# Kernel tuning notes

Hardware: AMD Instinct MI355X
Metric: run time of the kernel (lower is better)

The kernel has to match this reference:

```python
import jax, jax.numpy as jnp
import numpy as np

N_NODES = 100000
N_EDGES = 600000
D_IN = 128
D_OUT = 128

def gcn_conv(x, src, dst, W, b, n):
    # PyG GCNConv: h = X W; out_i = sum_j norm_ij * h_j + b, with self-loops and
    # symmetric normalization norm_ij = deg_i^{-1/2} deg_j^{-1/2}.
    deg = jax.ops.segment_sum(jnp.ones_like(dst, dtype=x.dtype), dst, num_segments=n)
    dinv = jnp.where(deg > 0, jax.lax.rsqrt(deg), 0.0)
    norm = dinv[src] * dinv[dst]            # [E]
    h = x @ W                                # [N, D_out]
    msg = h[src] * norm[:, None]             # gather + scale, [E, D_out]
    out = jax.ops.segment_sum(msg, dst, num_segments=n)
    return out + b

def setup_inputs() -> dict:
    key = jax.random.key(0)
    ks = jax.random.split(key, 8)
    x = jax.random.normal(ks[0], (N_NODES, D_IN), dtype=jnp.float32)
    edge_index = jax.random.randint(ks[1], (2, N_EDGES), 0, N_NODES, dtype=jnp.int64)
    s = (1.0 / np.sqrt(D_IN)).astype(np.float32) if isinstance(np.sqrt(D_IN), np.ndarray) else np.float32(1.0 / np.sqrt(D_IN))
    W1 = jax.random.normal(ks[2], (D_IN, D_OUT), dtype=jnp.float32) * s
    b1 = jnp.zeros((D_OUT,), dtype=jnp.float32)
    W2 = jax.random.normal(ks[3], (D_OUT, D_OUT), dtype=jnp.float32) * np.float32(1.0 / np.sqrt(D_OUT))
    b2 = jnp.zeros((D_OUT,), dtype=jnp.float32)
    Wfc = jax.random.normal(ks[4], (D_IN, D_OUT), dtype=jnp.float32) * s
    bfc = jnp.zeros((D_OUT,), dtype=jnp.float32)
    return {"x": x, "edge_index": edge_index, "W1": W1, "b1": b1,
            "W2": W2, "b2": b2, "Wfc": Wfc, "bfc": bfc}

def reference(x, edge_index, W1, b1, W2, b2, Wfc, bfc):
    n = x.shape[0]
    loop = jnp.arange(n, dtype=edge_index.dtype)
    src = jnp.concatenate([edge_index[0], loop])  # add self-loops
    dst = jnp.concatenate([edge_index[1], loop])
    res = x @ Wfc + bfc                           # linear residual branch
    h = jax.nn.relu(gcn_conv(x, src, dst, W1, b1, n))
    h = jax.nn.relu(gcn_conv(h, src, dst, W2, b2, n))
    return h + res
```

## Files before the change

### kernel.cpp

```cpp
#include <hip/hip_runtime.h>
#include <hip/hip_bf16.h>

#define D 128

typedef __bf16 bf16x8 __attribute__((ext_vector_type(8)));
typedef float f32x16 __attribute__((ext_vector_type(16)));

union U16 { uint4 u; bf16x8 v; };

static __device__ __forceinline__ unsigned short f2bf(float f) {
    unsigned u = __float_as_uint(f);
    unsigned r = (u + 0x7fffu + ((u >> 16) & 1u)) >> 16;
    return (unsigned short)r;
}
static __device__ __forceinline__ float bf2f(unsigned short s) {
    return __uint_as_float(((unsigned)s) << 16);
}
static __device__ __forceinline__ float u2f_lo(unsigned x) { return __uint_as_float(x << 16); }
static __device__ __forceinline__ float u2f_hi(unsigned x) { return __uint_as_float(x & 0xffff0000u); }


__global__ __launch_bounds__(256) void k_hist(const int* __restrict__ dst,
                                              int* __restrict__ cnt, int e) {
    int i = blockIdx.x * 256 + threadIdx.x;
    if (i < e) atomicAdd(&cnt[dst[i]], 1);
}

#define SCAN_CHUNK 1024

__global__ __launch_bounds__(256) void k_scan_local(const int* __restrict__ cnt,
                                                    int* __restrict__ ptr,
                                                    int* __restrict__ sums, int n) {
    __shared__ int tsum[256];
    const int t = threadIdx.x;
    const int base = blockIdx.x * SCAN_CHUNK + t * 4;
    int v[4]; int s = 0;
    #pragma unroll
    for (int i = 0; i < 4; ++i) {
        int idx = base + i;
        v[i] = (idx < n) ? cnt[idx] : 0;
        s += v[i];
    }
    tsum[t] = s;
    __syncthreads();
    for (int off = 1; off < 256; off <<= 1) {
        int x = (t >= off) ? tsum[t - off] : 0;
        __syncthreads();
        tsum[t] += x;
        __syncthreads();
    }
    int run = (t > 0) ? tsum[t - 1] : 0;
    if (t == 255) sums[blockIdx.x] = tsum[255];
    #pragma unroll
    for (int i = 0; i < 4; ++i) {
        int idx = base + i;
        if (idx < n) ptr[idx] = run;
        run += v[i];
    }
}

__global__ __launch_bounds__(256) void k_scan_sums(int* __restrict__ sums, int nChunks) {
    __shared__ int ls[256];
    const int t = threadIdx.x;
    ls[t] = (t < nChunks) ? sums[t] : 0;
    __syncthreads();
    for (int off = 1; off < 256; off <<= 1) {
        int x = (t >= off) ? ls[t - off] : 0;
        __syncthreads();
        ls[t] += x;
        __syncthreads();
    }
    if (t < nChunks) sums[t] = (t > 0) ? ls[t - 1] : 0;
}

__global__ __launch_bounds__(256) void k_scan_add(int* __restrict__ ptr,
                                                  const int* __restrict__ sums,
                                                  const int* __restrict__ cnt,
                                                  float* __restrict__ dinv,
                                                  int n, int e) {
    int i = blockIdx.x * 256 + threadIdx.x;
    if (i < n) {
        ptr[i] += sums[i >> 10];
        dinv[i] = rsqrtf((float)(1 + cnt[i]));
    }
    if (i == 0) ptr[n] = e;
}

__global__ __launch_bounds__(256) void k_fill(const int* __restrict__ src,
                                              const int* __restrict__ dst,
                                              const int* __restrict__ ptr,
                                              int* __restrict__ fill,
                                              int* __restrict__ csr_src, int e) {
    int i = blockIdx.x * 256 + threadIdx.x;
    if (i < e) {
        int d = dst[i];
        int slot = ptr[d] + atomicAdd(&fill[d], 1);
        csr_src[slot] = src[i];
    }
}

__global__ __launch_bounds__(256) void k_prep_w(const float* __restrict__ W,
                                                unsigned short* __restrict__ Wh,
                                                unsigned short* __restrict__ Wl) {
    int idx = blockIdx.x * 256 + threadIdx.x;
    int k = idx >> 7, n = idx & 127;
    float v = W[k * 128 + n];
    unsigned short h = f2bf(v);
    unsigned short l = f2bf(v - bf2f(h));
    Wh[n * 128 + k] = h;
    Wl[n * 128 + k] = l;
}

#define APAD 136

__global__ __launch_bounds__(256, 4) void k_gemm_rr(
        const float* __restrict__ A,
        const unsigned short* __restrict__ Bh, const unsigned short* __restrict__ Bl,
        const float* __restrict__ bias,
        unsigned short* __restrict__ outb,
        float* __restrict__ outf,
        int M, int nTiles) {
    __shared__ __align__(16) unsigned short As[2][32][APAD];

    const int tid = threadIdx.x;
    const int wave = tid >> 6;
    const int lane = tid & 63;
    const int l31 = lane & 31;
    const int quad8 = (lane >> 5) * 8;
    const int col = wave * 32 + l31;

    U16 bh[8], bl[8];
    #pragma unroll
    for (int ks = 0; ks < 8; ++ks) {
        const size_t bo = (size_t)col * D + ks * 16 + quad8;
        bh[ks].u = *(const uint4*)(Bh + bo);
        bl[ks].u = *(const uint4*)(Bl + bo);
    }
    const float bv = (bias != nullptr) ? bias[col] : 0.f;

    for (int t = blockIdx.x; t < nTiles; t += gridDim.x) {
        const int row0 = t * 32;

        #pragma unroll
        for (int i = 0; i < 4; ++i) {
            int f = tid + i * 256;
            int r = f >> 5, c4 = (f & 31) * 4;
            int rg = row0 + r; if (rg >= M) rg = M - 1;
            float4 v = *(const float4*)(A + (size_t)rg * D + c4);
            ushort4 hq, lq;
            hq.x = f2bf(v.x); hq.y = f2bf(v.y); hq.z = f2bf(v.z); hq.w = f2bf(v.w);
            lq.x = f2bf(v.x - bf2f(hq.x)); lq.y = f2bf(v.y - bf2f(hq.y));
            lq.z = f2bf(v.z - bf2f(hq.z)); lq.w = f2bf(v.w - bf2f(hq.w));
            *(ushort4*)&As[0][r][c4] = hq;
            *(ushort4*)&As[1][r][c4] = lq;
        }
        __syncthreads();

        f32x16 acc;
        #pragma unroll
        for (int r = 0; r < 16; ++r) acc[r] = 0.f;

        #pragma unroll
        for (int ks = 0; ks < 8; ++ks) {
            U16 ah, al;
            ah.u = *(const uint4*)&As[0][l31][ks * 16 + quad8];
            al.u = *(const uint4*)&As[1][l31][ks * 16 + quad8];
            acc = __builtin_amdgcn_mfma_f32_32x32x16_bf16(ah.v, bh[ks].v, acc, 0, 0, 0);
            acc = __builtin_amdgcn_mfma_f32_32x32x16_bf16(ah.v, bl[ks].v, acc, 0, 0, 0);
            acc = __builtin_amdgcn_mfma_f32_32x32x16_bf16(al.v, bh[ks].v, acc, 0, 0, 0);
        }
        __syncthreads();

        #pragma unroll
        for (int reg = 0; reg < 16; ++reg) {
            const int r = (reg & 3) + 8 * (reg >> 2) + 4 * (lane >> 5);
            const int rg = row0 + r;
            if (rg < M) {
                if (outb) outb[(size_t)rg * D + col] = f2bf(acc[reg]);
                else      outf[(size_t)rg * D + col] = acc[reg] + bv;
            }
        }
    }
}

__global__ __launch_bounds__(256) void k_gather_bf(const int* __restrict__ ptr,
                                                   const int* __restrict__ csr_src,
                                                   const float* __restrict__ dinv,
                                                   const unsigned short* __restrict__ h,
                                                   const float* __restrict__ bias,
                                                   const float* __restrict__ res,
                                                   float* __restrict__ out, int N) {
    const int g = threadIdx.x >> 5;
    const int lane = threadIdx.x & 31;
    const int i = blockIdx.x * 8 + g;
    if (i >= N) return;

    const int p0 = ptr[i];
    const int p1 = ptr[i + 1];
    const float di = dinv[i];

    float a0 = 0.f, a1 = 0.f, a2 = 0.f, a3 = 0.f;
    for (int j = p0; j < p1; ++j) {
        const int s = csr_src[j];
        const float c = dinv[s];
        const uint2 u = *(const uint2*)(h + (size_t)s * D + lane * 4);
        a0 = fmaf(c, u2f_lo(u.x), a0);
        a1 = fmaf(c, u2f_hi(u.x), a1);
        a2 = fmaf(c, u2f_lo(u.y), a2);
        a3 = fmaf(c, u2f_hi(u.y), a3);
    }

    const uint2 us = *(const uint2*)(h + (size_t)i * D + lane * 4);
    const float4 bv = *(const float4*)(bias + lane * 4);
    const float self = di * di;
    float4 o;
    o.x = fmaxf(di * a0 + self * u2f_lo(us.x) + bv.x, 0.0f);
    o.y = fmaxf(di * a1 + self * u2f_hi(us.x) + bv.y, 0.0f);
    o.z = fmaxf(di * a2 + self * u2f_lo(us.y) + bv.z, 0.0f);
    o.w = fmaxf(di * a3 + self * u2f_hi(us.y) + bv.w, 0.0f);
    if (res) {
        const float4 rv = *(const float4*)(res + (size_t)i * D + lane * 4);
        o.x += rv.x; o.y += rv.y; o.z += rv.z; o.w += rv.w;
    }
    *(float4*)(out + (size_t)i * D + lane * 4) = o;
}


extern "C" void kernel_launch(void* const* d_in, const int* in_sizes, int n_in,
                              void* d_out, int out_size, void* d_ws, size_t ws_size,
                              hipStream_t stream) {
    const int N = in_sizes[0] / D;
    const int E = in_sizes[1] / 2;

    const float* x   = (const float*)d_in[0];
    const int*   ei  = (const int*)d_in[1];
    const int*   src = ei;
    const int*   dst = ei + E;
    const float* W1  = (const float*)d_in[2];
    const float* b1  = (const float*)d_in[3];
    const float* W2  = (const float*)d_in[4];
    const float* b2  = (const float*)d_in[5];
    const float* Wfc = (const float*)d_in[6];
    const float* bfc = (const float*)d_in[7];
    float* out = (float*)d_out;

    char* ws = (char*)d_ws;
    size_t off = 0;
    auto alloc = [&](size_t bytes) { char* p = ws + off; off += (bytes + 255) & ~(size_t)255; return p; };
    float* dinv    = (float*)alloc((size_t)N * 4);
    int*   cnt     = (int*)  alloc((size_t)N * 4);
    int*   ptr     = (int*)  alloc((size_t)(N + 1) * 4);
    int*   sums    = (int*)  alloc(256 * 4);
    int*   csr_src = (int*)  alloc((size_t)E * 4);
    unsigned short* W1h = (unsigned short*)alloc(128 * 128 * 2);
    unsigned short* W1l = (unsigned short*)alloc(128 * 128 * 2);
    unsigned short* W2h = (unsigned short*)alloc(128 * 128 * 2);
    unsigned short* W2l = (unsigned short*)alloc(128 * 128 * 2);
    unsigned short* Wfh = (unsigned short*)alloc(128 * 128 * 2);
    unsigned short* Wfl = (unsigned short*)alloc(128 * 128 * 2);
    unsigned short* h   = (unsigned short*)alloc((size_t)N * D * 2);
    float* hb           = (float*)alloc((size_t)N * D * 4);

    const int nBlk    = (N + 255) / 256;
    const int eBlk    = (E + 255) / 256;
    const int aBlk    = (N + 7) / 8;
    const int nChunks = (N + SCAN_CHUNK - 1) / SCAN_CHUNK;
    const int nTiles  = (N + 31) / 32;
    const int gBlk    = nTiles < 1024 ? nTiles : 1024;

    k_prep_w<<<64, 256, 0, stream>>>(W1, W1h, W1l);
    k_prep_w<<<64, 256, 0, stream>>>(W2, W2h, W2l);
    k_prep_w<<<64, 256, 0, stream>>>(Wfc, Wfh, Wfl);

    hipMemsetAsync(cnt, 0, (size_t)N * 4, stream);
    k_hist<<<eBlk, 256, 0, stream>>>(dst, cnt, E);
    k_scan_local<<<nChunks, 256, 0, stream>>>(cnt, ptr, sums, N);
    k_scan_sums<<<1, 256, 0, stream>>>(sums, nChunks);
    k_scan_add<<<nBlk, 256, 0, stream>>>(ptr, sums, cnt, dinv, N, E);
    hipMemsetAsync(cnt, 0, (size_t)N * 4, stream);
    k_fill<<<eBlk, 256, 0, stream>>>(src, dst, ptr, cnt, csr_src, E);

    k_gemm_rr<<<gBlk, 256, 0, stream>>>(x, W1h, W1l, nullptr, h, nullptr, N, nTiles);
    k_gemm_rr<<<gBlk, 256, 0, stream>>>(x, Wfh, Wfl, bfc, nullptr, out, N, nTiles);

    k_gather_bf<<<aBlk, 256, 0, stream>>>(ptr, csr_src, dinv, h, b1, nullptr, hb, N);

    k_gemm_rr<<<gBlk, 256, 0, stream>>>(hb, W2h, W2l, nullptr, h, nullptr, N, nTiles);

    k_gather_bf<<<aBlk, 256, 0, stream>>>(ptr, csr_src, dinv, h, b2, out, out, N);
}
```

Before: 346.0 us.

## Store layer-1 activations in bf16, add bf16-input GEMM, unroll gather, fuse prep

The first gather now writes its ReLU output as bf16 instead of fp32, and a new GEMM kernel reads bf16 A directly. It does only two MFMAs per k-step (A times W-high and W-low), since A has no low-order split. The three weight-prep launches and the first memset are merged into one kernel, and the second memset becomes a zeroing step inside the scan-add kernel. The gather's edge loop is unrolled by 4 to keep more loads in flight. This cuts intermediate memory traffic and launch count, but layer-2 input precision drops to plain bf16.

```diff
diff --git a/kernel.cpp b/kernel.cpp
--- a/kernel.cpp
+++ b/kernel.cpp
@@ -18,6 +18,29 @@
 }
 static __device__ __forceinline__ float u2f_lo(unsigned x) { return __uint_as_float(x << 16); }
 static __device__ __forceinline__ float u2f_hi(unsigned x) { return __uint_as_float(x & 0xffff0000u); }
+
+__global__ __launch_bounds__(256) void k_prep(
+        const float* __restrict__ W1, const float* __restrict__ W2, const float* __restrict__ Wf,
+        unsigned short* __restrict__ W1h, unsigned short* __restrict__ W1l,
+        unsigned short* __restrict__ W2h, unsigned short* __restrict__ W2l,
+        unsigned short* __restrict__ Wfh, unsigned short* __restrict__ Wfl,
+        int* __restrict__ cnt, int n) {
+    int idx = blockIdx.x * 256 + threadIdx.x;
+    if (idx < 3 * 16384) {
+        int which = idx >> 14;
+        int local = idx & 16383;
+        int k = local >> 7, c = local & 127;
+        const float* W = (which == 0) ? W1 : (which == 1) ? W2 : Wf;
+        unsigned short* Wh = (which == 0) ? W1h : (which == 1) ? W2h : Wfh;
+        unsigned short* Wl = (which == 0) ? W1l : (which == 1) ? W2l : Wfl;
+        float v = W[k * 128 + c];
+        unsigned short h = f2bf(v);
+        unsigned short l = f2bf(v - bf2f(h));
+        Wh[c * 128 + k] = h;
+        Wl[c * 128 + k] = l;
+    }
+    if (idx < n) cnt[idx] = 0;
+}
 
 
 __global__ __launch_bounds__(256) void k_hist(const int* __restrict__ dst,
@@ -75,13 +98,14 @@
 
 __global__ __launch_bounds__(256) void k_scan_add(int* __restrict__ ptr,
                                                   const int* __restrict__ sums,
-                                                  const int* __restrict__ cnt,
+                                                  int* __restrict__ cnt,
                                                   float* __restrict__ dinv,
                                                   int n, int e) {
     int i = blockIdx.x * 256 + threadIdx.x;
     if (i < n) {
         ptr[i] += sums[i >> 10];
         dinv[i] = rsqrtf((float)(1 + cnt[i]));
+        cnt[i] = 0;
     }
     if (i == 0) ptr[n] = e;
 }
@@ -97,18 +121,6 @@
         int slot = ptr[d] + atomicAdd(&fill[d], 1);
         csr_src[slot] = src[i];
     }
-}
-
-__global__ __launch_bounds__(256) void k_prep_w(const float* __restrict__ W,
-                                                unsigned short* __restrict__ Wh,
-                                                unsigned short* __restrict__ Wl) {
-    int idx = blockIdx.x * 256 + threadIdx.x;
-    int k = idx >> 7, n = idx & 127;
-    float v = W[k * 128 + n];
-    unsigned short h = f2bf(v);
-    unsigned short l = f2bf(v - bf2f(h));
-    Wh[n * 128 + k] = h;
-    Wl[n * 128 + k] = l;
 }
 
 #define APAD 136
@@ -183,13 +195,71 @@
     }
 }
 
+__global__ __launch_bounds__(256, 4) void k_gemm_rr_bf(
+        const unsigned short* __restrict__ A,
+        const unsigned short* __restrict__ Bh, const unsigned short* __restrict__ Bl,
+        unsigned short* __restrict__ outb,
+        int M, int nTiles) {
+    __shared__ __align__(16) unsigned short As[32][APAD];
+
+    const int tid = threadIdx.x;
+    const int wave = tid >> 6;
+    const int lane = tid & 63;
+    const int l31 = lane & 31;
+    const int quad8 = (lane >> 5) * 8;
+    const int col = wave * 32 + l31;
+
+    U16 bh[8], bl[8];
+    #pragma unroll
+    for (int ks = 0; ks < 8; ++ks) {
+        const size_t bo = (size_t)col * D + ks * 16 + quad8;
+        bh[ks].u = *(const uint4*)(Bh + bo);
+        bl[ks].u = *(const uint4*)(Bl + bo);
+    }
+
+    for (int t = blockIdx.x; t < nTiles; t += gridDim.x) {
+        const int row0 = t * 32;
+
+        #pragma unroll
+        for (int i = 0; i < 2; ++i) {
+            int f = tid + i * 256;
+            int r = f >> 4, c8 = (f & 15) * 8;
+            int rg = row0 + r; if (rg >= M) rg = M - 1;
+            *(uint4*)&As[r][c8] = *(const uint4*)(A + (size_t)rg * D + c8);
+        }
+        __syncthreads();
+
+        f32x16 acc;
+        #pragma unroll
+        for (int r = 0; r < 16; ++r) acc[r] = 0.f;
+
+        #pragma unroll
+        for (int ks = 0; ks < 8; ++ks) {
+            U16 ah;
+            ah.u = *(const uint4*)&As[l31][ks * 16 + quad8];
+            acc = __builtin_amdgcn_mfma_f32_32x32x16_bf16(ah.v, bh[ks].v, acc, 0, 0, 0);
+            acc = __builtin_amdgcn_mfma_f32_32x32x16_bf16(ah.v, bl[ks].v, acc, 0, 0, 0);
+        }
+        __syncthreads();
+
+        #pragma unroll
+        for (int reg = 0; reg < 16; ++reg) {
+            const int r = (reg & 3) + 8 * (reg >> 2) + 4 * (lane >> 5);
+            const int rg = row0 + r;
+            if (rg < M) outb[(size_t)rg * D + col] = f2bf(acc[reg]);
+        }
+    }
+}
+
 __global__ __launch_bounds__(256) void k_gather_bf(const int* __restrict__ ptr,
                                                    const int* __restrict__ csr_src,
                                                    const float* __restrict__ dinv,
                                                    const unsigned short* __restrict__ h,
                                                    const float* __restrict__ bias,
                                                    const float* __restrict__ res,
-                                                   float* __restrict__ out, int N) {
+                                                   float* __restrict__ outf,
+                                                   unsigned short* __restrict__ outb,
+                                                   int N) {
     const int g = threadIdx.x >> 5;
     const int lane = threadIdx.x & 31;
     const int i = blockIdx.x * 8 + g;
@@ -200,7 +270,27 @@
     const float di = dinv[i];
 
     float a0 = 0.f, a1 = 0.f, a2 = 0.f, a3 = 0.f;
-    for (int j = p0; j < p1; ++j) {
+    int j = p0;
+    for (; j + 4 <= p1; j += 4) {
+        const int s0 = csr_src[j + 0];
+        const int s1 = csr_src[j + 1];
+        const int s2 = csr_src[j + 2];
+        const int s3 = csr_src[j + 3];
+        const float c0 = dinv[s0], c1 = dinv[s1], c2 = dinv[s2], c3 = dinv[s3];
+        const uint2 u0 = *(const uint2*)(h + (size_t)s0 * D + lane * 4);
+        const uint2 u1 = *(const uint2*)(h + (size_t)s1 * D + lane * 4);
+        const uint2 u2 = *(const uint2*)(h + (size_t)s2 * D + lane * 4);
+        const uint2 u3 = *(const uint2*)(h + (size_t)s3 * D + lane * 4);
+        a0 = fmaf(c0, u2f_lo(u0.x), a0); a1 = fmaf(c0, u2f_hi(u0.x), a1);
+        a2 = fmaf(c0, u2f_lo(u0.y), a2); a3 = fmaf(c0, u2f_hi(u0.y), a3);
+        a0 = fmaf(c1, u2f_lo(u1.x), a0); a1 = fmaf(c1, u2f_hi(u1.x), a1);
+        a2 = fmaf(c1, u2f_lo(u1.y), a2); a3 = fmaf(c1, u2f_hi(u1.y), a3);
+        a0 = fmaf(c2, u2f_lo(u2.x), a0); a1 = fmaf(c2, u2f_hi(u2.x), a1);
+        a2 = fmaf(c2, u2f_lo(u2.y), a2); a3 = fmaf(c2, u2f_hi(u2.y), a3);
+        a0 = fmaf(c3, u2f_lo(u3.x), a0); a1 = fmaf(c3, u2f_hi(u3.x), a1);
+        a2 = fmaf(c3, u2f_lo(u3.y), a2); a3 = fmaf(c3, u2f_hi(u3.y), a3);
+    }
+    for (; j < p1; ++j) {
         const int s = csr_src[j];
         const float c = dinv[s];
         const uint2 u = *(const uint2*)(h + (size_t)s * D + lane * 4);
@@ -213,16 +303,21 @@
     const uint2 us = *(const uint2*)(h + (size_t)i * D + lane * 4);
     const float4 bv = *(const float4*)(bias + lane * 4);
     const float self = di * di;
-    float4 o;
-    o.x = fmaxf(di * a0 + self * u2f_lo(us.x) + bv.x, 0.0f);
-    o.y = fmaxf(di * a1 + self * u2f_hi(us.x) + bv.y, 0.0f);
-    o.z = fmaxf(di * a2 + self * u2f_lo(us.y) + bv.z, 0.0f);
-    o.w = fmaxf(di * a3 + self * u2f_hi(us.y) + bv.w, 0.0f);
-    if (res) {
-        const float4 rv = *(const float4*)(res + (size_t)i * D + lane * 4);
-        o.x += rv.x; o.y += rv.y; o.z += rv.z; o.w += rv.w;
-    }
-    *(float4*)(out + (size_t)i * D + lane * 4) = o;
+    float o0 = fmaxf(di * a0 + self * u2f_lo(us.x) + bv.x, 0.0f);
+    float o1 = fmaxf(di * a1 + self * u2f_hi(us.x) + bv.y, 0.0f);
+    float o2 = fmaxf(di * a2 + self * u2f_lo(us.y) + bv.z, 0.0f);
+    float o3 = fmaxf(di * a3 + self * u2f_hi(us.y) + bv.w, 0.0f);
+    if (outb) {
+        ushort4 q = {f2bf(o0), f2bf(o1), f2bf(o2), f2bf(o3)};
+        *(ushort4*)(outb + (size_t)i * D + lane * 4) = q;
+    } else {
+        if (res) {
+            const float4 rv = *(const float4*)(res + (size_t)i * D + lane * 4);
+            o0 += rv.x; o1 += rv.y; o2 += rv.z; o3 += rv.w;
+        }
+        float4 o = {o0, o1, o2, o3};
+        *(float4*)(outf + (size_t)i * D + lane * 4) = o;
+    }
 }
 
 
@@ -258,8 +353,8 @@
     unsigned short* W2l = (unsigned short*)alloc(128 * 128 * 2);
     unsigned short* Wfh = (unsigned short*)alloc(128 * 128 * 2);
     unsigned short* Wfl = (unsigned short*)alloc(128 * 128 * 2);
-    unsigned short* h   = (unsigned short*)alloc((size_t)N * D * 2);
-    float* hb           = (float*)alloc((size_t)N * D * 4);
+    unsigned short* h    = (unsigned short*)alloc((size_t)N * D * 2);
+    unsigned short* hb16 = (unsigned short*)alloc((size_t)N * D * 2);
 
     const int nBlk    = (N + 255) / 256;
     const int eBlk    = (E + 255) / 256;
@@ -267,25 +362,22 @@
     const int nChunks = (N + SCAN_CHUNK - 1) / SCAN_CHUNK;
     const int nTiles  = (N + 31) / 32;
     const int gBlk    = nTiles < 1024 ? nTiles : 1024;
-
-    k_prep_w<<<64, 256, 0, stream>>>(W1, W1h, W1l);
-    k_prep_w<<<64, 256, 0, stream>>>(W2, W2h, W2l);
-    k_prep_w<<<64, 256, 0, stream>>>(Wfc, Wfh, Wfl);
-
-    hipMemsetAsync(cnt, 0, (size_t)N * 4, stream);
+    const int pBlk    = (nBlk > 192) ? nBlk : 192;
+
+    k_prep<<<pBlk, 256, 0, stream>>>(W1, W2, Wfc, W1h, W1l, W2h, W2l, Wfh, Wfl, cnt, N);
+
     k_hist<<<eBlk, 256, 0, stream>>>(dst, cnt, E);
     k_scan_local<<<nChunks, 256, 0, stream>>>(cnt, ptr, sums, N);
     k_scan_sums<<<1, 256, 0, stream>>>(sums, nChunks);
     k_scan_add<<<nBlk, 256, 0, stream>>>(ptr, sums, cnt, dinv, N, E);
-    hipMemsetAsync(cnt, 0, (size_t)N * 4, stream);
     k_fill<<<eBlk, 256, 0, stream>>>(src, dst, ptr, cnt, csr_src, E);
 
     k_gemm_rr<<<gBlk, 256, 0, stream>>>(x, W1h, W1l, nullptr, h, nullptr, N, nTiles);
     k_gemm_rr<<<gBlk, 256, 0, stream>>>(x, Wfh, Wfl, bfc, nullptr, out, N, nTiles);
 
-    k_gather_bf<<<aBlk, 256, 0, stream>>>(ptr, csr_src, dinv, h, b1, nullptr, hb, N);
-
-    k_gemm_rr<<<gBlk, 256, 0, stream>>>(hb, W2h, W2l, nullptr, h, nullptr, N, nTiles);
-
-    k_gather_bf<<<aBlk, 256, 0, stream>>>(ptr, csr_src, dinv, h, b2, out, out, N);
-}
+    k_gather_bf<<<aBlk, 256, 0, stream>>>(ptr, csr_src, dinv, h, b1, nullptr, nullptr, hb16, N);
+
+    k_gemm_rr_bf<<<gBlk, 256, 0, stream>>>(hb16, W2h, W2l, h, N, nTiles);
+
+    k_gather_bf<<<aBlk, 256, 0, stream>>>(ptr, csr_src, dinv, h, b2, out, out, nullptr, N);
+}
```

Result: faster. 304.6 us (-12.0%).
